# Optimization experiments

Measured on AMD Instinct MI355X. Metric: run time of the kernel, lower is better.

Reference implementation:

```python
import jax, jax.numpy as jnp
import numpy as np

N, P, S, CORE, H, HEADS, B = 49152, 256, 256, 192, 256, 8, 1
D = H // HEADS  # head_dim = 32
EPS = 1e-5


def setup_inputs() -> dict:
    key = jax.random.key(0)
    ks = jax.random.split(key, 8)
    x = jax.random.normal(ks[0], (B, N, H), dtype=jnp.float32)
    # cores tile all N nodes exactly once (KMeans-like partition), plus random overlap ring
    core = jnp.arange(N, dtype=jnp.int32).reshape(P, CORE)
    ov = jax.random.randint(ks[1], (P, S - CORE), 0, N, dtype=jnp.int32)
    patch_idx = jnp.concatenate([core, ov], axis=1)                      # [P,S]
    core_mask = jnp.concatenate(
        [jnp.ones((P, CORE), bool), jnp.zeros((P, S - CORE), bool)], axis=1)  # [P,S]
    def w(k):
        return jax.random.normal(k, (H, H), dtype=jnp.float32) * 0.02
    return dict(
        x=x, patch_idx=patch_idx, core_mask=core_mask,
        Wq=w(ks[2]), bq=jnp.zeros((H,), jnp.float32),
        Wk=w(ks[3]), bk=jnp.zeros((H,), jnp.float32),
        Wv=w(ks[4]), bv=jnp.zeros((H,), jnp.float32),
        Wo=w(ks[5]), bo=jnp.zeros((H,), jnp.float32),
        ln_g=jnp.ones((H,), jnp.float32), ln_b=jnp.zeros((H,), jnp.float32),
    )


def reference(x, patch_idx, core_mask, Wq, bq, Wk, bk, Wv, bv, Wo, bo, ln_g, ln_b):
    # x: [B,N,H]; patch_idx: [P,S] int; core_mask: [P,S] bool
    px = x[:, patch_idx]                                   # gather -> [B,P,S,H]
    def proj(W, b):
        return (px @ W.T + b).reshape(B, P, S, HEADS, D)
    Q, K, V = proj(Wq, bq), proj(Wk, bk), proj(Wv, bv)
    scores = jnp.einsum('bpihd,bpjhd->bphij', Q, K) / jnp.sqrt(jnp.float32(D))
    attn = jax.nn.softmax(scores, axis=-1)                 # dropout is identity in eval
    att = jnp.einsum('bphij,bpjhd->bpihd', attn, V).reshape(B, P, S, H)
    out = att @ Wo.T + bo                                  # [B,P,S,H]
    # scatter-add only core slots back to nodes, track update counts
    contrib = jnp.where(core_mask[None, :, :, None], out, 0.0).reshape(B, P * S, H)
    flat = patch_idx.reshape(-1)
    acc = jnp.zeros((B, N, H), x.dtype).at[:, flat].add(contrib)
    cnt = jnp.zeros((N,), x.dtype).at[flat].add(core_mask.reshape(-1).astype(x.dtype))
    acc = acc / jnp.clip(cnt, 1.0)[None, :, None]
    # residual + LayerNorm (biased variance, as torch)
    y = x + acc
    mu = jnp.mean(y, axis=-1, keepdims=True)
    var = jnp.var(y, axis=-1, keepdims=True)
    return (y - mu) / jnp.sqrt(var + EPS) * ln_g + ln_b
```

## Files before the change

kernel.cpp:

```cpp
#include <hip/hip_runtime.h>

#define PP 256
#define SS 256
#define CORE_ 192
#define HH 256
#define NHEAD 8
#define DD 32

typedef __attribute__((ext_vector_type(4))) float f32x4;
typedef __attribute__((ext_vector_type(8))) short s8v;
typedef __attribute__((ext_vector_type(4))) short s4v;

__device__ __forceinline__ float bf2f(unsigned short u) {
    union { unsigned int i; float f; } c; c.i = ((unsigned int)u) << 16; return c.f;
}
__device__ __forceinline__ unsigned short f2bf(float f) {
    union { float f; unsigned int i; } c; c.f = f;
    unsigned int i = c.i;
    return (unsigned short)((i + 0x7fffu + ((i >> 16) & 1u)) >> 16);
}

__device__ __forceinline__ void gload16(const unsigned short* g, unsigned short* l) {
    __builtin_amdgcn_global_load_lds(
        (const __attribute__((address_space(1))) void*)g,
        (__attribute__((address_space(3))) void*)l, 16, 0, 0);
}

#define SW(row, chunk) ((chunk) ^ (((row) >> 1) & 3))
__device__ __forceinline__ int swcol(int c, int row) {
    return (c & ~31) | (((((c >> 3) & 3) ^ ((row >> 1) & 3))) << 3) | (c & 7);
}

__global__ __launch_bounds__(256) void k_prep(
    const float* __restrict__ Wq, const float* __restrict__ Wk,
    const float* __restrict__ Wv, const float* __restrict__ Wo,
    const float* __restrict__ bq, const float* __restrict__ bk,
    const float* __restrict__ bv,
    unsigned short* __restrict__ Wb, float* __restrict__ bb) {
    int bid = blockIdx.x, tid = threadIdx.x;
    if (bid >= 128) {
        int which = bid - 128;
        const float* b = which == 0 ? bq : which == 1 ? bk : bv;
        bb[which * 256 + tid] = b[tid];
        return;
    }
    int c = bid * 256 + tid;
    int row = c >> 5;
    int within = c & 31;
    int w = within >> 2, sl = within & 3;
    const float* src = row < 256 ? Wq : row < 512 ? Wk : row < 768 ? Wv : Wo;
    const float* sp = src + (size_t)(row & 255) * 256 + w * 32 + SW(row, sl) * 8;
    float4 a = *(const float4*)sp;
    float4 b4 = *(const float4*)(sp + 4);
    s8v wv;
    wv[0] = (short)f2bf(a.x); wv[1] = (short)f2bf(a.y);
    wv[2] = (short)f2bf(a.z); wv[3] = (short)f2bf(a.w);
    wv[4] = (short)f2bf(b4.x); wv[5] = (short)f2bf(b4.y);
    wv[6] = (short)f2bf(b4.z); wv[7] = (short)f2bf(b4.w);
    *(s8v*)(Wb + (size_t)row * 256 + w * 32 + sl * 8) = wv;
}

__global__ __launch_bounds__(256) void k_qkv(
    const float* __restrict__ x, const int* __restrict__ pidx,
    const unsigned short* __restrict__ Wb, const float* __restrict__ bb,
    unsigned short* __restrict__ qkv) {
    int bx = blockIdx.x, p = blockIdx.y;
    int mt = bx / 3, ng = bx % 3;
    if (ng == 0 && mt == 3) return;
    __shared__ unsigned short As[64][32];
    __shared__ unsigned short Bs[256][32];
    int tid = threadIdx.x;
    int wave = tid >> 6, lane = tid & 63;
    int g = lane >> 4, c0 = lane & 15;
    f32x4 acc[4][4] = {};
    int arow = tid >> 2, aseg = tid & 3;
    int node = pidx[p * SS + mt * 64 + arow];
    const float* asrc = x + (size_t)node * HH + aseg * 8;
    const unsigned short* wsrc = Wb + (size_t)ng * 256 * 256;

    float4 v0 = *(const float4*)(asrc);
    float4 v1 = *(const float4*)(asrc + 4);
#pragma unroll
    for (int ks = 0; ks < 8; ++ks) {
        int k0 = ks * 32;
#pragma unroll
        for (int j = 0; j < 4; ++j) {
            int chunk = j * 256 + wave * 64 + lane;
            int row = chunk >> 2, c8 = chunk & 3;
            gload16(wsrc + (size_t)row * 256 + k0 + c8 * 8,
                    &Bs[0][0] + (size_t)(j * 256 + wave * 64) * 8);
        }
        s8v aw;
        aw[0] = (short)f2bf(v0.x); aw[1] = (short)f2bf(v0.y);
        aw[2] = (short)f2bf(v0.z); aw[3] = (short)f2bf(v0.w);
        aw[4] = (short)f2bf(v1.x); aw[5] = (short)f2bf(v1.y);
        aw[6] = (short)f2bf(v1.z); aw[7] = (short)f2bf(v1.w);
        *(s8v*)&As[arow][SW(arow, aseg) * 8] = aw;
        if (ks < 7) {
            v0 = *(const float4*)(asrc + k0 + 32);
            v1 = *(const float4*)(asrc + k0 + 36);
        }
        __syncthreads();
        s8v af[4], bfv[4];
#pragma unroll
        for (int m2 = 0; m2 < 4; ++m2) {
            int r = m2 * 16 + c0;
            af[m2] = *(const s8v*)&As[r][SW(r, g) * 8];
        }
#pragma unroll
        for (int nt = 0; nt < 4; ++nt) {
            int r = wave * 64 + nt * 16 + c0;
            bfv[nt] = *(const s8v*)&Bs[r][SW(r, g) * 8];
        }
#pragma unroll
        for (int m2 = 0; m2 < 4; ++m2)
#pragma unroll
            for (int nt = 0; nt < 4; ++nt)
                acc[m2][nt] = __builtin_amdgcn_mfma_f32_16x16x32_bf16(
                    af[m2], bfv[nt], acc[m2][nt], 0, 0, 0);
        __syncthreads();
    }
#pragma unroll
    for (int nt = 0; nt < 4; ++nt) {
        int ncol = wave * 64 + nt * 16 + c0;
        float bv_ = bb[ng * 256 + ncol];
#pragma unroll
        for (int m2 = 0; m2 < 4; ++m2)
#pragma unroll
            for (int r = 0; r < 4; ++r) {
                int srow = mt * 64 + m2 * 16 + g * 4 + r;
                int sc = (ng == 1) ? swcol(ncol, srow) : ncol;
                qkv[((size_t)p * SS + srow) * 768 + ng * 256 + sc] =
                    f2bf(acc[m2][nt][r] + bv_);
            }
    }
}

__global__ __launch_bounds__(256) void k_attn(
    const unsigned short* __restrict__ qkv, unsigned short* __restrict__ att) {
    int p = blockIdx.x, h = blockIdx.y;
    __shared__ unsigned short Ks[256][32];
    __shared__ unsigned short Vt[32][256];
    __shared__ unsigned short Pb[4][16][128];
    int tid = threadIdx.x;
    int wave = tid >> 6, lane = tid & 63;
    int g = lane >> 4, c0 = lane & 15;

#pragma unroll
    for (int j = 0; j < 4; ++j) {
        int chunk = j * 256 + wave * 64 + lane;
        int row = chunk >> 2, c8 = chunk & 3;
        gload16(qkv + ((size_t)p * SS + row) * 768 + 256 + h * DD + c8 * 8,
                &Ks[0][0] + (size_t)(j * 256 + wave * 64) * 8);
    }
    {
        int dw = tid & 3, jb = tid >> 2;
        int j0 = jb * 4;
        const unsigned short* vbase =
            qkv + ((size_t)p * SS + j0) * 768 + 512 + h * DD + dw * 8;
        s8v r0 = *(const s8v*)(vbase);
        s8v r1 = *(const s8v*)(vbase + 768);
        s8v r2 = *(const s8v*)(vbase + 1536);
        s8v r3 = *(const s8v*)(vbase + 2304);
        int cj = j0 >> 3, jo = j0 & 7;
#pragma unroll
        for (int e = 0; e < 8; ++e) {
            int d = dw * 8 + e;
            s4v w4;
            w4[0] = r0[e]; w4[1] = r1[e]; w4[2] = r2[e]; w4[3] = r3[e];
            *(s4v*)&Vt[d][((cj ^ ((d >> 1) & 7)) << 3) + jo] = w4;
        }
    }
    __syncthreads();

    const float C2 = 0.2550348792930095f;
    int cs = (c0 >> 1) & 7;

    for (int mi = 0; mi < 3; ++mi) {
        int q0 = (wave * 3 + mi) * 16;
        s8v qa = *(const s8v*)(qkv + ((size_t)p * SS + q0 + c0) * 768 + h * DD + g * 8);
        f32x4 sacc[16];
#pragma unroll
        for (int jt = 0; jt < 16; ++jt) {
            int row = jt * 16 + c0;
            s8v kf = *(const s8v*)&Ks[row][SW(row, g) * 8];
            sacc[jt] = __builtin_amdgcn_mfma_f32_16x16x32_bf16(
                qa, kf, f32x4{0.f, 0.f, 0.f, 0.f}, 0, 0, 0);
        }
        float mx[4], sum[4], linv[4];
#pragma unroll
        for (int r = 0; r < 4; ++r) mx[r] = sacc[0][r];
#pragma unroll
        for (int jt = 1; jt < 16; ++jt)
#pragma unroll
            for (int r = 0; r < 4; ++r) mx[r] = fmaxf(mx[r], sacc[jt][r]);
#pragma unroll
        for (int off = 1; off < 16; off <<= 1)
#pragma unroll
            for (int r = 0; r < 4; ++r)
                mx[r] = fmaxf(mx[r], __shfl_xor(mx[r], off, 64));
#pragma unroll
        for (int r = 0; r < 4; ++r) sum[r] = 0.f;
#pragma unroll
        for (int jt = 0; jt < 16; ++jt)
#pragma unroll
            for (int r = 0; r < 4; ++r) {
                float e = exp2f((sacc[jt][r] - mx[r]) * C2);
                sacc[jt][r] = e;
                sum[r] += e;
            }
#pragma unroll
        for (int off = 1; off < 16; off <<= 1)
#pragma unroll
            for (int r = 0; r < 4; ++r)
                sum[r] += __shfl_xor(sum[r], off, 64);
#pragma unroll
        for (int r = 0; r < 4; ++r) linv[r] = 1.f / sum[r];

        f32x4 oacc[2] = {f32x4{0.f, 0.f, 0.f, 0.f}, f32x4{0.f, 0.f, 0.f, 0.f}};
#pragma unroll
        for (int half = 0; half < 2; ++half) {
#pragma unroll
            for (int r = 0; r < 4; ++r) {
                int qq = g * 4 + r, qs = (qq >> 1) & 7;
                unsigned short* prow = &Pb[wave][qq][0];
#pragma unroll
                for (int jt = 0; jt < 8; ++jt) {
                    int j0 = jt * 2 + (c0 >> 3);
                    prow[((j0 ^ qs) << 3) + (c0 & 7)] =
                        (unsigned short)f2bf(sacc[half * 8 + jt][r]);
                }
            }
            asm volatile("s_waitcnt lgkmcnt(0)" ::: "memory");
            __builtin_amdgcn_sched_barrier(0);
#pragma unroll
            for (int kt = 0; kt < 4; ++kt) {
                int ktg = half * 4 + kt;
                s8v pa = *(const s8v*)&Pb[wave][c0][(((kt * 4 + g) ^ cs) << 3)];
#pragma unroll
                for (int nt = 0; nt < 2; ++nt) {
                    int d = nt * 16 + c0;
                    s8v vb = *(const s8v*)&Vt[d][(((ktg * 4 + g) ^ ((d >> 1) & 7)) << 3)];
                    oacc[nt] = __builtin_amdgcn_mfma_f32_16x16x32_bf16(
                        pa, vb, oacc[nt], 0, 0, 0);
                }
            }
            asm volatile("s_waitcnt lgkmcnt(0)" ::: "memory");
            __builtin_amdgcn_sched_barrier(0);
        }
#pragma unroll
        for (int nt = 0; nt < 2; ++nt)
#pragma unroll
            for (int r = 0; r < 4; ++r) {
                int qq = g * 4 + r;
                int crow = q0 + qq;
                int c = h * DD + nt * 16 + c0;
                att[((size_t)p * CORE_ + crow) * HH + swcol(c, crow)] =
                    f2bf(oacc[nt][r] * linv[r]);
            }
    }
}

__global__ __launch_bounds__(256) void k_out(
    const unsigned short* __restrict__ att, const float* __restrict__ x,
    const unsigned short* __restrict__ Wb, const float* __restrict__ bo,
    const float* __restrict__ ln_g, const float* __restrict__ ln_b,
    float* __restrict__ out) {
    int p = blockIdx.x, mb = blockIdx.y;
    __shared__ unsigned short As[2][64][32];
    __shared__ unsigned short Bs[2][256][32];
    int tid = threadIdx.x;
    int wave = tid >> 6, lane = tid & 63;
    int g = lane >> 4, c0 = lane & 15;
    f32x4 acc[16] = {};

    auto stage = [&](int k0, int b) {
        {
            int chunk = wave * 64 + lane;
            int row = chunk >> 2, c8 = chunk & 3;
            gload16(att + ((size_t)p * CORE_ + mb * 64 + row) * HH + k0 + c8 * 8,
                    &As[b][0][0] + (size_t)(wave * 64) * 8);
        }
#pragma unroll
        for (int j = 0; j < 4; ++j) {
            int chunk = j * 256 + wave * 64 + lane;
            int row = chunk >> 2, c8 = chunk & 3;
            gload16(Wb + (size_t)(768 + row) * 256 + k0 + c8 * 8,
                    &Bs[b][0][0] + (size_t)(j * 256 + wave * 64) * 8);
        }
    };

    stage(0, 0);
    __syncthreads();
#pragma unroll
    for (int ks = 0; ks < 8; ++ks) {
        int b = ks & 1;
        if (ks < 7) stage((ks + 1) * 32, b ^ 1);
        int ar = wave * 16 + c0;
        s8v af = *(const s8v*)&As[b][ar][SW(ar, g) * 8];
#pragma unroll
        for (int nt = 0; nt < 16; ++nt) {
            int r = nt * 16 + c0;
            s8v bfv = *(const s8v*)&Bs[b][r][SW(r, g) * 8];
            acc[nt] = __builtin_amdgcn_mfma_f32_16x16x32_bf16(af, bfv, acc[nt], 0, 0, 0);
        }
        __syncthreads();
    }
    int srow0 = mb * 64 + wave * 16 + g * 4;
    float sum[4] = {0, 0, 0, 0}, ssq[4] = {0, 0, 0, 0};
#pragma unroll
    for (int nt = 0; nt < 16; ++nt) {
        int col = nt * 16 + c0;
        float bov = bo[col];
#pragma unroll
        for (int r = 0; r < 4; ++r) {
            size_t node = (size_t)p * CORE_ + srow0 + r;
            float v = acc[nt][r] + bov + x[node * HH + col];
            acc[nt][r] = v;
            sum[r] += v; ssq[r] += v * v;
        }
    }
#pragma unroll
    for (int off = 1; off < 16; off <<= 1) {
#pragma unroll
        for (int r = 0; r < 4; ++r) {
            sum[r] += __shfl_xor(sum[r], off, 64);
            ssq[r] += __shfl_xor(ssq[r], off, 64);
        }
    }
#pragma unroll
    for (int r = 0; r < 4; ++r) {
        float mu = sum[r] * (1.f / HH);
        float var = ssq[r] * (1.f / HH) - mu * mu;
        float rstd = rsqrtf(var + 1e-5f);
        size_t node = (size_t)p * CORE_ + srow0 + r;
#pragma unroll
        for (int nt = 0; nt < 16; ++nt) {
            int col = nt * 16 + c0;
            out[node * HH + col] = (acc[nt][r] - mu) * rstd * ln_g[col] + ln_b[col];
        }
    }
}

extern "C" void kernel_launch(void* const* d_in, const int* in_sizes, int n_in,
                              void* d_out, int out_size, void* d_ws, size_t ws_size,
                              hipStream_t stream) {
    const float* x   = (const float*)d_in[0];
    const int* pidx  = (const int*)d_in[1];
    const float* Wq  = (const float*)d_in[3];
    const float* bq  = (const float*)d_in[4];
    const float* Wk  = (const float*)d_in[5];
    const float* bk  = (const float*)d_in[6];
    const float* Wv  = (const float*)d_in[7];
    const float* bv  = (const float*)d_in[8];
    const float* Wo  = (const float*)d_in[9];
    const float* bo  = (const float*)d_in[10];
    const float* lng = (const float*)d_in[11];
    const float* lnb = (const float*)d_in[12];

    unsigned short* qkv = (unsigned short*)d_ws;
    unsigned short* att = qkv + (size_t)PP * SS * 768;
    unsigned short* Wb  = att + (size_t)PP * CORE_ * HH;
    float* bb = (float*)(Wb + 1024 * 256);

    k_prep<<<131, 256, 0, stream>>>(Wq, Wk, Wv, Wo, bq, bk, bv, Wb, bb);
    k_qkv<<<dim3(12, PP), 256, 0, stream>>>(x, pidx, Wb, bb, qkv);
    k_attn<<<dim3(PP, NHEAD), 256, 0, stream>>>(qkv, att);
    k_out<<<dim3(PP, 3), 256, 0, stream>>>(att, x, Wb, bo, lng, lnb, (float*)d_out);
}
```

Before: 162.5 us.

## Fuse attention with output projection and LayerNorm in one per-patch kernel

Merges the per-(patch,head) attention kernel and the output-projection+LayerNorm kernel into a single 512-thread kernel per patch that loops over heads. Each head's attention output stays in shared memory and is accumulated straight into Wo-projection registers, so the att intermediate is never written to or read from global memory. Idle waves in the second round do part of the projection MMAs, and LayerNorm statistics are reduced across waves through shared memory. The k_qkv grid is also reordered so the patch index varies fastest. The cost is only 256 blocks with heavy register use (launch_bounds 512,1) and serialized head iterations with extra barriers, which lowers occupancy and parallelism.

```diff
diff --git a/kernel.cpp b/kernel.cpp
--- a/kernel.cpp
+++ b/kernel.cpp
@@ -11,9 +11,6 @@
 typedef __attribute__((ext_vector_type(8))) short s8v;
 typedef __attribute__((ext_vector_type(4))) short s4v;
 
-__device__ __forceinline__ float bf2f(unsigned short u) {
-    union { unsigned int i; float f; } c; c.i = ((unsigned int)u) << 16; return c.f;
-}
 __device__ __forceinline__ unsigned short f2bf(float f) {
     union { float f; unsigned int i; } c; c.f = f;
     unsigned int i = c.i;
@@ -64,8 +61,7 @@
     const float* __restrict__ x, const int* __restrict__ pidx,
     const unsigned short* __restrict__ Wb, const float* __restrict__ bb,
     unsigned short* __restrict__ qkv) {
-    int bx = blockIdx.x, p = blockIdx.y;
-    int mt = bx / 3, ng = bx % 3;
+    int p = blockIdx.x, mt = blockIdx.y, ng = blockIdx.z;
     if (ng == 0 && mt == 3) return;
     __shared__ unsigned short As[64][32];
     __shared__ unsigned short Bs[256][32];
@@ -136,210 +132,213 @@
     }
 }
 
-__global__ __launch_bounds__(256) void k_attn(
-    const unsigned short* __restrict__ qkv, unsigned short* __restrict__ att) {
-    int p = blockIdx.x, h = blockIdx.y;
-    __shared__ unsigned short Ks[256][32];
-    __shared__ unsigned short Vt[32][256];
-    __shared__ unsigned short Pb[4][16][128];
-    int tid = threadIdx.x;
-    int wave = tid >> 6, lane = tid & 63;
-    int g = lane >> 4, c0 = lane & 15;
-
-#pragma unroll
-    for (int j = 0; j < 4; ++j) {
-        int chunk = j * 256 + wave * 64 + lane;
-        int row = chunk >> 2, c8 = chunk & 3;
-        gload16(qkv + ((size_t)p * SS + row) * 768 + 256 + h * DD + c8 * 8,
-                &Ks[0][0] + (size_t)(j * 256 + wave * 64) * 8);
-    }
-    {
-        int dw = tid & 3, jb = tid >> 2;
-        int j0 = jb * 4;
-        const unsigned short* vbase =
-            qkv + ((size_t)p * SS + j0) * 768 + 512 + h * DD + dw * 8;
-        s8v r0 = *(const s8v*)(vbase);
-        s8v r1 = *(const s8v*)(vbase + 768);
-        s8v r2 = *(const s8v*)(vbase + 1536);
-        s8v r3 = *(const s8v*)(vbase + 2304);
-        int cj = j0 >> 3, jo = j0 & 7;
-#pragma unroll
-        for (int e = 0; e < 8; ++e) {
-            int d = dw * 8 + e;
-            s4v w4;
-            w4[0] = r0[e]; w4[1] = r1[e]; w4[2] = r2[e]; w4[3] = r3[e];
-            *(s4v*)&Vt[d][((cj ^ ((d >> 1) & 7)) << 3) + jo] = w4;
-        }
-    }
-    __syncthreads();
-
-    const float C2 = 0.2550348792930095f;
-    int cs = (c0 >> 1) & 7;
-
-    for (int mi = 0; mi < 3; ++mi) {
-        int q0 = (wave * 3 + mi) * 16;
-        s8v qa = *(const s8v*)(qkv + ((size_t)p * SS + q0 + c0) * 768 + h * DD + g * 8);
-        f32x4 sacc[16];
-#pragma unroll
-        for (int jt = 0; jt < 16; ++jt) {
-            int row = jt * 16 + c0;
-            s8v kf = *(const s8v*)&Ks[row][SW(row, g) * 8];
-            sacc[jt] = __builtin_amdgcn_mfma_f32_16x16x32_bf16(
-                qa, kf, f32x4{0.f, 0.f, 0.f, 0.f}, 0, 0, 0);
-        }
-        float mx[4], sum[4], linv[4];
-#pragma unroll
-        for (int r = 0; r < 4; ++r) mx[r] = sacc[0][r];
-#pragma unroll
-        for (int jt = 1; jt < 16; ++jt)
-#pragma unroll
-            for (int r = 0; r < 4; ++r) mx[r] = fmaxf(mx[r], sacc[jt][r]);
-#pragma unroll
-        for (int off = 1; off < 16; off <<= 1)
-#pragma unroll
-            for (int r = 0; r < 4; ++r)
-                mx[r] = fmaxf(mx[r], __shfl_xor(mx[r], off, 64));
-#pragma unroll
-        for (int r = 0; r < 4; ++r) sum[r] = 0.f;
-#pragma unroll
-        for (int jt = 0; jt < 16; ++jt)
-#pragma unroll
-            for (int r = 0; r < 4; ++r) {
-                float e = exp2f((sacc[jt][r] - mx[r]) * C2);
-                sacc[jt][r] = e;
-                sum[r] += e;
-            }
-#pragma unroll
-        for (int off = 1; off < 16; off <<= 1)
-#pragma unroll
-            for (int r = 0; r < 4; ++r)
-                sum[r] += __shfl_xor(sum[r], off, 64);
-#pragma unroll
-        for (int r = 0; r < 4; ++r) linv[r] = 1.f / sum[r];
-
-        f32x4 oacc[2] = {f32x4{0.f, 0.f, 0.f, 0.f}, f32x4{0.f, 0.f, 0.f, 0.f}};
-#pragma unroll
-        for (int half = 0; half < 2; ++half) {
-#pragma unroll
-            for (int r = 0; r < 4; ++r) {
-                int qq = g * 4 + r, qs = (qq >> 1) & 7;
-                unsigned short* prow = &Pb[wave][qq][0];
-#pragma unroll
-                for (int jt = 0; jt < 8; ++jt) {
-                    int j0 = jt * 2 + (c0 >> 3);
-                    prow[((j0 ^ qs) << 3) + (c0 & 7)] =
-                        (unsigned short)f2bf(sacc[half * 8 + jt][r]);
-                }
-            }
-            asm volatile("s_waitcnt lgkmcnt(0)" ::: "memory");
-            __builtin_amdgcn_sched_barrier(0);
-#pragma unroll
-            for (int kt = 0; kt < 4; ++kt) {
-                int ktg = half * 4 + kt;
-                s8v pa = *(const s8v*)&Pb[wave][c0][(((kt * 4 + g) ^ cs) << 3)];
-#pragma unroll
-                for (int nt = 0; nt < 2; ++nt) {
-                    int d = nt * 16 + c0;
-                    s8v vb = *(const s8v*)&Vt[d][(((ktg * 4 + g) ^ ((d >> 1) & 7)) << 3)];
-                    oacc[nt] = __builtin_amdgcn_mfma_f32_16x16x32_bf16(
-                        pa, vb, oacc[nt], 0, 0, 0);
-                }
-            }
-            asm volatile("s_waitcnt lgkmcnt(0)" ::: "memory");
-            __builtin_amdgcn_sched_barrier(0);
-        }
-#pragma unroll
-        for (int nt = 0; nt < 2; ++nt)
-#pragma unroll
-            for (int r = 0; r < 4; ++r) {
-                int qq = g * 4 + r;
-                int crow = q0 + qq;
-                int c = h * DD + nt * 16 + c0;
-                att[((size_t)p * CORE_ + crow) * HH + swcol(c, crow)] =
-                    f2bf(oacc[nt][r] * linv[r]);
-            }
-    }
-}
-
-__global__ __launch_bounds__(256) void k_out(
-    const unsigned short* __restrict__ att, const float* __restrict__ x,
+__global__ __launch_bounds__(512, 1) void k_attno(
+    const unsigned short* __restrict__ qkv, const float* __restrict__ x,
     const unsigned short* __restrict__ Wb, const float* __restrict__ bo,
     const float* __restrict__ ln_g, const float* __restrict__ ln_b,
     float* __restrict__ out) {
-    int p = blockIdx.x, mb = blockIdx.y;
-    __shared__ unsigned short As[2][64][32];
-    __shared__ unsigned short Bs[2][256][32];
+    int p = blockIdx.x;
+    __shared__ unsigned short Ks[256][32];
+    __shared__ unsigned short Vt[32][256];
+    __shared__ unsigned short Ah[192][32];
+    __shared__ unsigned short Pb[8][16][64];
     int tid = threadIdx.x;
     int wave = tid >> 6, lane = tid & 63;
-    int g = lane >> 4, c0 = lane & 15;
-    f32x4 acc[16] = {};
-
-    auto stage = [&](int k0, int b) {
+    int g = (lane >> 4) & 3, c0 = lane & 15;
+    const float C2 = 0.2550348792930095f;
+    int cs = (c0 >> 1) & 7;
+
+    f32x4 oc[12][2] = {};
+
+    for (int h = 0; h < NHEAD; ++h) {
+#pragma unroll
+        for (int j = 0; j < 2; ++j) {
+            int chunk = j * 512 + wave * 64 + lane;
+            int row = chunk >> 2, c8 = chunk & 3;
+            gload16(qkv + ((size_t)p * SS + row) * 768 + 256 + h * DD + c8 * 8,
+                    &Ks[0][0] + (size_t)(j * 512 + wave * 64) * 8);
+        }
         {
-            int chunk = wave * 64 + lane;
-            int row = chunk >> 2, c8 = chunk & 3;
-            gload16(att + ((size_t)p * CORE_ + mb * 64 + row) * HH + k0 + c8 * 8,
-                    &As[b][0][0] + (size_t)(wave * 64) * 8);
-        }
-#pragma unroll
-        for (int j = 0; j < 4; ++j) {
-            int chunk = j * 256 + wave * 64 + lane;
-            int row = chunk >> 2, c8 = chunk & 3;
-            gload16(Wb + (size_t)(768 + row) * 256 + k0 + c8 * 8,
-                    &Bs[b][0][0] + (size_t)(j * 256 + wave * 64) * 8);
-        }
-    };
-
-    stage(0, 0);
+            int dw = tid & 3, jb = tid >> 2;
+            int j0 = jb * 2;
+            const unsigned short* vb0 =
+                qkv + ((size_t)p * SS + j0) * 768 + 512 + h * DD + dw * 8;
+            s8v r0 = *(const s8v*)(vb0);
+            s8v r1 = *(const s8v*)(vb0 + 768);
+            int cj = j0 >> 3, jo = j0 & 7;
+#pragma unroll
+            for (int e = 0; e < 8; ++e) {
+                int d = dw * 8 + e;
+                unsigned int pr = ((unsigned int)(unsigned short)r0[e]) |
+                                  (((unsigned int)(unsigned short)r1[e]) << 16);
+                *(unsigned int*)&Vt[d][((cj ^ ((d >> 1) & 7)) << 3) + jo] = pr;
+            }
+        }
+        int wr0 = 768 + wave * 32 + c0;
+        int wr1 = wr0 + 16;
+        s8v wo0 = *(const s8v*)(Wb + (size_t)wr0 * 256 + h * DD + SW(wr0, g) * 8);
+        s8v wo1 = *(const s8v*)(Wb + (size_t)wr1 * 256 + h * DD + SW(wr1, g) * 8);
+        __syncthreads();
+
+        for (int rd = 0; rd < 2; ++rd) {
+            int mi = rd * 8 + wave;
+            if (mi < 12) {
+                int q0 = mi * 16;
+                s8v qa = *(const s8v*)(qkv + ((size_t)p * SS + q0 + c0) * 768 +
+                                       h * DD + g * 8);
+                f32x4 sacc[16];
+#pragma unroll
+                for (int jt = 0; jt < 16; ++jt) {
+                    int row = jt * 16 + c0;
+                    s8v kf = *(const s8v*)&Ks[row][SW(row, g) * 8];
+                    sacc[jt] = __builtin_amdgcn_mfma_f32_16x16x32_bf16(
+                        qa, kf, f32x4{0.f, 0.f, 0.f, 0.f}, 0, 0, 0);
+                }
+                float mx[4], sm[4], linv[4];
+#pragma unroll
+                for (int r = 0; r < 4; ++r) mx[r] = sacc[0][r];
+#pragma unroll
+                for (int jt = 1; jt < 16; ++jt)
+#pragma unroll
+                    for (int r = 0; r < 4; ++r) mx[r] = fmaxf(mx[r], sacc[jt][r]);
+#pragma unroll
+                for (int off = 1; off < 16; off <<= 1)
+#pragma unroll
+                    for (int r = 0; r < 4; ++r)
+                        mx[r] = fmaxf(mx[r], __shfl_xor(mx[r], off, 64));
+#pragma unroll
+                for (int r = 0; r < 4; ++r) sm[r] = 0.f;
+#pragma unroll
+                for (int jt = 0; jt < 16; ++jt)
+#pragma unroll
+                    for (int r = 0; r < 4; ++r) {
+                        float e = exp2f((sacc[jt][r] - mx[r]) * C2);
+                        sacc[jt][r] = e;
+                        sm[r] += e;
+                    }
+#pragma unroll
+                for (int off = 1; off < 16; off <<= 1)
+#pragma unroll
+                    for (int r = 0; r < 4; ++r)
+                        sm[r] += __shfl_xor(sm[r], off, 64);
+#pragma unroll
+                for (int r = 0; r < 4; ++r) linv[r] = 1.f / sm[r];
+
+                f32x4 oacc[2] = {f32x4{0.f, 0.f, 0.f, 0.f},
+                                 f32x4{0.f, 0.f, 0.f, 0.f}};
+#pragma unroll
+                for (int qu = 0; qu < 4; ++qu) {
+#pragma unroll
+                    for (int r = 0; r < 4; ++r) {
+                        int qr = g * 4 + r, qs = (qr >> 1) & 7;
+                        unsigned short* prow = &Pb[wave][qr][0];
+#pragma unroll
+                        for (int jq = 0; jq < 4; ++jq) {
+                            int lc = jq * 2 + (c0 >> 3);
+                            prow[((lc ^ qs) << 3) + (c0 & 7)] =
+                                (unsigned short)f2bf(sacc[qu * 4 + jq][r]);
+                        }
+                    }
+                    asm volatile("s_waitcnt lgkmcnt(0)" ::: "memory");
+                    __builtin_amdgcn_sched_barrier(0);
+#pragma unroll
+                    for (int kt = 0; kt < 2; ++kt) {
+                        int ktg = qu * 2 + kt;
+                        s8v pa = *(const s8v*)&Pb[wave][c0][(((kt * 4 + g) ^ cs) << 3)];
+#pragma unroll
+                        for (int nt = 0; nt < 2; ++nt) {
+                            int d = nt * 16 + c0;
+                            s8v vb = *(const s8v*)&Vt[d]
+                                [(((ktg * 4 + g) ^ ((d >> 1) & 7)) << 3)];
+                            oacc[nt] = __builtin_amdgcn_mfma_f32_16x16x32_bf16(
+                                pa, vb, oacc[nt], 0, 0, 0);
+                        }
+                    }
+                    asm volatile("s_waitcnt lgkmcnt(0)" ::: "memory");
+                    __builtin_amdgcn_sched_barrier(0);
+                }
+#pragma unroll
+                for (int nt = 0; nt < 2; ++nt)
+#pragma unroll
+                    for (int r = 0; r < 4; ++r) {
+                        int row = q0 + g * 4 + r;
+                        int ch = nt * 2 + (c0 >> 3);
+                        Ah[row][SW(row, ch) * 8 + (c0 & 7)] =
+                            (unsigned short)f2bf(oacc[nt][r] * linv[r]);
+                    }
+            } else {
+#pragma unroll
+                for (int m = 0; m < 8; ++m) {
+                    int ar = m * 16 + c0;
+                    s8v af = *(const s8v*)&Ah[ar][SW(ar, g) * 8];
+                    oc[m][0] = __builtin_amdgcn_mfma_f32_16x16x32_bf16(
+                        af, wo0, oc[m][0], 0, 0, 0);
+                    oc[m][1] = __builtin_amdgcn_mfma_f32_16x16x32_bf16(
+                        af, wo1, oc[m][1], 0, 0, 0);
+                }
+            }
+            __syncthreads();
+        }
+        int m0 = (wave < 4) ? 0 : 8;
+#pragma unroll
+        for (int m = 0; m < 12; ++m) {
+            if (m < m0) continue;
+            int ar = m * 16 + c0;
+            s8v af = *(const s8v*)&Ah[ar][SW(ar, g) * 8];
+            oc[m][0] = __builtin_amdgcn_mfma_f32_16x16x32_bf16(
+                af, wo0, oc[m][0], 0, 0, 0);
+            oc[m][1] = __builtin_amdgcn_mfma_f32_16x16x32_bf16(
+                af, wo1, oc[m][1], 0, 0, 0);
+        }
+        __syncthreads();
+    }
+
+    float* Ps  = (float*)&Pb[0][0][0];
+    float* Ps2 = Ps + 192 * 8;
+    float bo0 = bo[wave * 32 + c0];
+    float bo1 = bo[wave * 32 + 16 + c0];
+    float lg0 = ln_g[wave * 32 + c0], lg1 = ln_g[wave * 32 + 16 + c0];
+    float lb0 = ln_b[wave * 32 + c0], lb1 = ln_b[wave * 32 + 16 + c0];
+#pragma unroll
+    for (int m = 0; m < 12; ++m)
+#pragma unroll
+        for (int r = 0; r < 4; ++r) {
+            int row = m * 16 + g * 4 + r;
+            const float* xr = x + ((size_t)p * CORE_ + row) * HH + wave * 32;
+            float v0 = oc[m][0][r] + bo0 + xr[c0];
+            float v1 = oc[m][1][r] + bo1 + xr[16 + c0];
+            oc[m][0][r] = v0; oc[m][1][r] = v1;
+            float s = v0 + v1, q = v0 * v0 + v1 * v1;
+#pragma unroll
+            for (int off = 1; off < 16; off <<= 1) {
+                s += __shfl_xor(s, off, 64);
+                q += __shfl_xor(q, off, 64);
+            }
+            if (c0 == 0) { Ps[row * 8 + wave] = s; Ps2[row * 8 + wave] = q; }
+        }
     __syncthreads();
-#pragma unroll
-    for (int ks = 0; ks < 8; ++ks) {
-        int b = ks & 1;
-        if (ks < 7) stage((ks + 1) * 32, b ^ 1);
-        int ar = wave * 16 + c0;
-        s8v af = *(const s8v*)&As[b][ar][SW(ar, g) * 8];
-#pragma unroll
-        for (int nt = 0; nt < 16; ++nt) {
-            int r = nt * 16 + c0;
-            s8v bfv = *(const s8v*)&Bs[b][r][SW(r, g) * 8];
-            acc[nt] = __builtin_amdgcn_mfma_f32_16x16x32_bf16(af, bfv, acc[nt], 0, 0, 0);
-        }
-        __syncthreads();
-    }
-    int srow0 = mb * 64 + wave * 16 + g * 4;
-    float sum[4] = {0, 0, 0, 0}, ssq[4] = {0, 0, 0, 0};
-#pragma unroll
-    for (int nt = 0; nt < 16; ++nt) {
-        int col = nt * 16 + c0;
-        float bov = bo[col];
+    float* Mu = (float*)&Ah[0][0];
+    float* Rs = Mu + 192;
+    if (tid < 192) {
+        float s = 0.f, q = 0.f;
+#pragma unroll
+        for (int w = 0; w < 8; ++w) { s += Ps[tid * 8 + w]; q += Ps2[tid * 8 + w]; }
+        float mu = s * (1.f / 256.f);
+        float var = q * (1.f / 256.f) - mu * mu;
+        Mu[tid] = mu;
+        Rs[tid] = rsqrtf(var + 1e-5f);
+    }
+    __syncthreads();
+#pragma unroll
+    for (int m = 0; m < 12; ++m)
 #pragma unroll
         for (int r = 0; r < 4; ++r) {
-            size_t node = (size_t)p * CORE_ + srow0 + r;
-            float v = acc[nt][r] + bov + x[node * HH + col];
-            acc[nt][r] = v;
-            sum[r] += v; ssq[r] += v * v;
-        }
-    }
-#pragma unroll
-    for (int off = 1; off < 16; off <<= 1) {
-#pragma unroll
-        for (int r = 0; r < 4; ++r) {
-            sum[r] += __shfl_xor(sum[r], off, 64);
-            ssq[r] += __shfl_xor(ssq[r], off, 64);
-        }
-    }
-#pragma unroll
-    for (int r = 0; r < 4; ++r) {
-        float mu = sum[r] * (1.f / HH);
-        float var = ssq[r] * (1.f / HH) - mu * mu;
-        float rstd = rsqrtf(var + 1e-5f);
-        size_t node = (size_t)p * CORE_ + srow0 + r;
-#pragma unroll
-        for (int nt = 0; nt < 16; ++nt) {
-            int col = nt * 16 + c0;
-            out[node * HH + col] = (acc[nt][r] - mu) * rstd * ln_g[col] + ln_b[col];
-        }
-    }
+            int row = m * 16 + g * 4 + r;
+            float mu = Mu[row], rs = Rs[row];
+            float* orow = out + ((size_t)p * CORE_ + row) * HH + wave * 32;
+            orow[c0]      = (oc[m][0][r] - mu) * rs * lg0 + lb0;
+            orow[16 + c0] = (oc[m][1][r] - mu) * rs * lg1 + lb1;
+        }
 }
 
 extern "C" void kernel_launch(void* const* d_in, const int* in_sizes, int n_in,
@@ -359,12 +358,10 @@
     const float* lnb = (const float*)d_in[12];
 
     unsigned short* qkv = (unsigned short*)d_ws;
-    unsigned short* att = qkv + (size_t)PP * SS * 768;
-    unsigned short* Wb  = att + (size_t)PP * CORE_ * HH;
+    unsigned short* Wb  = qkv + (size_t)PP * SS * 768;
     float* bb = (float*)(Wb + 1024 * 256);
 
     k_prep<<<131, 256, 0, stream>>>(Wq, Wk, Wv, Wo, bq, bk, bv, Wb, bb);
-    k_qkv<<<dim3(12, PP), 256, 0, stream>>>(x, pidx, Wb, bb, qkv);
-    k_attn<<<dim3(PP, NHEAD), 256, 0, stream>>>(qkv, att);
-    k_out<<<dim3(PP, 3), 256, 0, stream>>>(att, x, Wb, bo, lng, lnb, (float*)d_out);
-}
+    k_qkv<<<dim3(PP, 4, 3), 256, 0, stream>>>(x, pidx, Wb, bb, qkv);
+    k_attno<<<PP, 512, 0, stream>>>(qkv, x, Wb, bo, lng, lnb, (float*)d_out);
+}
```

Result: slower. 175.6 us (+8.0%).
